# Kernel tuning notes

Measured on AMD Instinct MI355X. Metric: run time of the kernel, lower is better.

The kernel has to match this reference:

```python
import jax, jax.numpy as jnp
import numpy as np

B, N0, D, H = 64, 512, 512, 2048  # graphs, nodes/graph, d_hidden, mlp hidden


def _mlp(x, W1, b1, W2, b2, W3, b3):
    h = jax.nn.relu(x @ W1 + b1)
    h = jax.nn.relu(h @ W2 + b2)
    return h @ W3 + b3


def setup_inputs() -> dict:
    key = jax.random.key(0)
    ks = jax.random.split(key, 16)
    total = B * N0
    x = jax.random.normal(ks[0], (total, D), jnp.float32)
    node_type = jax.random.randint(ks[1], (total,), 0, 4, jnp.int32)
    action_mask = jax.random.bernoulli(ks[2], 0.5, (total,))
    node_indices = jnp.tile(jnp.arange(N0, dtype=jnp.int32), B)
    batch = jnp.repeat(jnp.arange(B, dtype=jnp.int32), N0)
    N = jnp.full((B,), N0, dtype=jnp.int32)

    def lin(k, fan_in, fan_out):
        kw, kb = jax.random.split(k)
        bound = 1.0 / np.sqrt(fan_in)
        W = jax.random.uniform(kw, (fan_in, fan_out), jnp.float32, -bound, bound)
        b = jax.random.uniform(kb, (fan_out,), jnp.float32, -bound, bound)
        return W, b

    mlp_W1, mlp_b1 = lin(ks[3], D, H)
    mlp_W2, mlp_b2 = lin(ks[4], H, H)
    mlp_W3, mlp_b3 = lin(ks[5], H, 1)
    vf_W1, vf_b1 = lin(ks[6], D, H)
    vf_W2, vf_b2 = lin(ks[7], H, H)
    vf_W3, vf_b3 = lin(ks[8], H, 1)
    return dict(x=x, node_type=node_type, action_mask=action_mask,
                node_indices=node_indices, batch=batch, N=N,
                mlp_W1=mlp_W1, mlp_b1=mlp_b1, mlp_W2=mlp_W2, mlp_b2=mlp_b2,
                mlp_W3=mlp_W3, mlp_b3=mlp_b3,
                vf_W1=vf_W1, vf_b1=vf_b1, vf_W2=vf_W2, vf_b2=vf_b2,
                vf_W3=vf_W3, vf_b3=vf_b3)


def reference(x, node_type, action_mask, node_indices, batch, N,
              mlp_W1, mlp_b1, mlp_W2, mlp_b2, mlp_W3, mlp_b3,
              vf_W1, vf_b1, vf_W2, vf_b2, vf_W3, vf_b3):
    nb = N.shape[0]
    # global mean pool over graphs
    counts = jax.ops.segment_sum(jnp.ones((x.shape[0],), x.dtype), batch, num_segments=nb)
    h_mean = jax.ops.segment_sum(x, batch, num_segments=nb) / counts[:, None]
    # masked gather -> MLP -> scatter with -inf fill, expressed as masked select
    z_node = _mlp(x, mlp_W1, mlp_b1, mlp_W2, mlp_b2, mlp_W3, mlp_b3)[:, 0]
    z_all = jnp.where(action_mask, z_node, -jnp.inf)
    z = z_all.reshape(nb, -1)  # multi_length=False: all graphs have N[0] nodes
    v = _mlp(h_mean, vf_W1, vf_b1, vf_W2, vf_b2, vf_W3, vf_b3)
    return z, v
```

## Files before the change

kernel.cpp:

```cpp
#include <hip/hip_runtime.h>
#include <cstdint>
#include <cmath>


typedef __bf16 bf16_t;
typedef float  f32x4  __attribute__((ext_vector_type(4)));
typedef int    i32x4  __attribute__((ext_vector_type(4)));
typedef int    i32x8  __attribute__((ext_vector_type(8)));

#define NB      64
#define N0      512
#define DIM     512
#define HID     2048
#define TOTAL   32768
#define ZNEG    -3.0e38f

__device__ __forceinline__ void gload16(const void* g, void* l) {
  __builtin_amdgcn_global_load_lds(
      (const uint32_t __attribute__((address_space(1)))*)g,
      (uint32_t __attribute__((address_space(3)))*)l, 16, 0, 0);
}

__device__ __forceinline__ unsigned char to_fp8(float f) {
  return (unsigned char)(__builtin_amdgcn_cvt_pk_fp8_f32(f, f, 0, false) & 0xff);
}

__global__ void mask_scan_kernel(const unsigned char* __restrict__ mask,
                                 int* __restrict__ perm,
                                 int* __restrict__ pos,
                                 int* __restrict__ mcount) {
  __shared__ int ts[1024];
  const int t = threadIdx.x;
  const uint32_t* m32 = (const uint32_t*)mask;
  uint32_t w[8];
  int s = 0;
#pragma unroll
  for (int k = 0; k < 8; ++k) {
    w[k] = m32[t * 8 + k];
    s += __popc(w[k] & 0x01010101u);
  }
  ts[t] = s;
  __syncthreads();
  for (int off = 1; off < 1024; off <<= 1) {
    int v = (t >= off) ? ts[t - off] : 0;
    __syncthreads();
    ts[t] += v;
    __syncthreads();
  }
  int run = ts[t] - s;
  const int base = t * 32;
#pragma unroll
  for (int k = 0; k < 32; ++k) {
    int bit = (w[k >> 2] >> ((k & 3) * 8)) & 1;
    if (bit) {
      perm[run] = base + k;
      pos[base + k] = run;
      run++;
    }
  }
  if (t == 1023) {
    mcount[0] = ts[1023];
    mcount[1] = (ts[1023] + 127) & ~127;
  }
}

__global__ void gather_fp8_kernel(const float* __restrict__ x,
                                  const int* __restrict__ perm,
                                  const int* __restrict__ mcount,
                                  uint32_t* __restrict__ xc) {
  const int idx = blockIdx.x * 256 + threadIdx.x;
  const int r = idx >> 7;
  const int c = idx & 127;
  if (r >= mcount[1]) return;
  uint32_t v = 0;
  if (r < mcount[0]) {
    const float4 f = ((const float4*)(x + (size_t)perm[r] * DIM))[c];
    int p = __builtin_amdgcn_cvt_pk_fp8_f32(f.x, f.y, 0, false);
    p = __builtin_amdgcn_cvt_pk_fp8_f32(f.z, f.w, p, true);
    v = (uint32_t)p;
  }
  xc[idx] = v;
}


__global__ void transpose_to_fp8_kernel(const float* __restrict__ W,
                                        uint8_t* __restrict__ Wt,
                                        int K, int N, float scale) {
  __shared__ float tile[32][33];
  const int bx = blockIdx.x;
  const int by = blockIdx.y;
  const int tx = threadIdx.x & 31;
  const int ty = threadIdx.x >> 5;
#pragma unroll
  for (int r = 0; r < 4; ++r)
    tile[ty + r * 8][tx] = W[(size_t)(by * 32 + ty + r * 8) * N + bx * 32 + tx];
  __syncthreads();
#pragma unroll
  for (int r = 0; r < 4; ++r)
    Wt[(size_t)(bx * 32 + ty + r * 8) * K + by * 32 + tx] =
        to_fp8(tile[tx][ty + r * 8] * scale);
}

__global__ void zero_kernel(float* __restrict__ p, int n) {
  int i = blockIdx.x * 256 + threadIdx.x;
  if (i < n) p[i] = 0.f;
}

__global__ void hmean_accum_kernel(const float* __restrict__ x,
                                   float* __restrict__ hsumT) {
  const int g = blockIdx.x >> 3;
  const int slab = blockIdx.x & 7;
  const int c = threadIdx.x;
  const float* xp = x + ((size_t)g * N0 + slab * 64) * DIM + c;
  float s = 0.f;
#pragma unroll 8
  for (int r = 0; r < 64; ++r) s += xp[(size_t)r * DIM];
  atomicAdd(&hsumT[(size_t)c * NB + g], s);
}

__global__ void vf_partial_kernel(const float* __restrict__ h,
                                  const float* __restrict__ W,
                                  float* __restrict__ pacc,
                                  int kspan) {
  const int tx = threadIdx.x & 31;
  const int ty = threadIdx.x >> 5;
  const int n  = blockIdx.x * 32 + tx;
  const int g0 = ty * 8;
  const int k0 = blockIdx.y * kspan;
  float acc[8] = {};
  const float* wp = W + (size_t)k0 * HID + n;
  const float* hp = h + (size_t)k0 * NB + g0;
#pragma unroll 8
  for (int kk = 0; kk < kspan; ++kk) {
    float w = wp[(size_t)kk * HID];
    float4 h0 = *(const float4*)(hp + kk * NB);
    float4 h1 = *(const float4*)(hp + kk * NB + 4);
    acc[0] += h0.x * w; acc[1] += h0.y * w;
    acc[2] += h0.z * w; acc[3] += h0.w * w;
    acc[4] += h1.x * w; acc[5] += h1.y * w;
    acc[6] += h1.z * w; acc[7] += h1.w * w;
  }
#pragma unroll
  for (int r = 0; r < 8; ++r)
    pacc[((size_t)blockIdx.y * NB + g0 + r) * HID + n] = acc[r];
}

__global__ void vf_l1_fin_kernel(const float* __restrict__ pacc1,
                                 const float* __restrict__ vb1,
                                 float* __restrict__ vh1t) {
  const int idx = blockIdx.x * 256 + threadIdx.x;
  const int g = idx >> 11;
  const int n = idx & 2047;
  float s = 0.f;
#pragma unroll
  for (int kg = 0; kg < 8; ++kg)
    s += pacc1[((size_t)kg * NB + g) * HID + n];
  vh1t[(size_t)n * NB + g] = fmaxf(s * (1.f / 512.f) + vb1[n], 0.f);
}

__global__ void vf_l23_fin_kernel(const float* __restrict__ pacc2,
                                  const float* __restrict__ vb2,
                                  const float* __restrict__ vW3,
                                  float* __restrict__ vfzp) {
  __shared__ float rs[4];
  const int g = blockIdx.x >> 3;
  const int n = (blockIdx.x & 7) * 256 + threadIdx.x;
  float s = 0.f;
#pragma unroll
  for (int kg = 0; kg < 16; ++kg)
    s += pacc2[((size_t)kg * NB + g) * HID + n];
  float t = fmaxf(s + vb2[n], 0.f) * vW3[n];
#pragma unroll
  for (int off = 32; off; off >>= 1) t += __shfl_down(t, off, 64);
  if ((threadIdx.x & 63) == 0) rs[threadIdx.x >> 6] = t;
  __syncthreads();
  if (threadIdx.x == 0)
    vfzp[g * 8 + (blockIdx.x & 7)] = rs[0] + rs[1] + rs[2] + rs[3];
}

template <int FUSE>
__global__ __launch_bounds__(256) void gemm_f8(
    const uint8_t* __restrict__ A, const uint8_t* __restrict__ Bt,
    const float* __restrict__ bias, const float* __restrict__ w3,
    uint8_t* __restrict__ C, float* __restrict__ zout,
    const int* __restrict__ mlim, int M, int N, int K, int sb) {
  const int bm = blockIdx.y;
  const int bn = blockIdx.x;
  if (bm * 128 >= *mlim) return;

  __shared__ __align__(16) char Asb[128 * 128];
  __shared__ __align__(16) char Bsb[128 * 128];

  const int tid = threadIdx.x;
  const int wave = tid >> 6;
  const int lane = tid & 63;
  const int lr = lane & 15;
  const int lq = lane >> 4;
  const int swz = lr & 7;
  const int wm = (wave >> 1) << 6;
  const int wn = (wave & 1) << 6;

  const int srow0 = (wave << 3) + (lane >> 3);
  const int gchunk = (lane & 7) ^ (lane >> 3);

  const uint8_t* ag = A + (size_t)(bm * 128 + srow0) * K + (gchunk << 4);
  const uint8_t* bg = Bt + (size_t)(bn * 128 + srow0) * K + (gchunk << 4);
  char* asw = Asb + (wave << 10);
  char* bsw = Bsb + (wave << 10);

  f32x4 acc[4][4] = {};

  for (int k0 = 0; k0 < K; k0 += 128) {
#pragma unroll
    for (int j = 0; j < 4; ++j) {
      gload16(ag + (size_t)(j * 32) * K, asw + j * 4096);
      gload16(bg + (size_t)(j * 32) * K, bsw + j * 4096);
    }
    ag += 128;
    bg += 128;
    __syncthreads();

    i32x8 a8[4], b8[4];
#pragma unroll
    for (int i = 0; i < 4; ++i) {
      const char* base = Asb + ((wm + i * 16 + lr) << 7);
      i32x4 lo = *(const i32x4*)(base + ((((lq << 1) | 0) ^ swz) << 4));
      i32x4 hi = *(const i32x4*)(base + ((((lq << 1) | 1) ^ swz) << 4));
      a8[i] = __builtin_shufflevector(lo, hi, 0, 1, 2, 3, 4, 5, 6, 7);
    }
#pragma unroll
    for (int j = 0; j < 4; ++j) {
      const char* base = Bsb + ((wn + j * 16 + lr) << 7);
      i32x4 lo = *(const i32x4*)(base + ((((lq << 1) | 0) ^ swz) << 4));
      i32x4 hi = *(const i32x4*)(base + ((((lq << 1) | 1) ^ swz) << 4));
      b8[j] = __builtin_shufflevector(lo, hi, 0, 1, 2, 3, 4, 5, 6, 7);
    }
#pragma unroll
    for (int i = 0; i < 4; ++i)
#pragma unroll
      for (int j = 0; j < 4; ++j)
        acc[i][j] = __builtin_amdgcn_mfma_scale_f32_16x16x128_f8f6f4(
            a8[i], b8[j], acc[i][j], 0 , 0 ,
            0, 127 , 0, sb);
    __syncthreads();
  }

  if (FUSE == 0) {
#pragma unroll
    for (int j = 0; j < 4; ++j) {
      const int gc = bn * 128 + wn + j * 16 + lr;
      const float bj = bias[gc];
#pragma unroll
      for (int i = 0; i < 4; ++i) {
        const int gr0 = bm * 128 + wm + i * 16 + lq * 4;
#pragma unroll
        for (int r = 0; r < 4; ++r) {
          float v = fmaxf(acc[i][j][r] + bj, 0.f);
          C[(size_t)(gr0 + r) * N + gc] = to_fp8(v);
        }
      }
    }
  } else {
    float rs[4][4] = {};
#pragma unroll
    for (int j = 0; j < 4; ++j) {
      const int gc = bn * 128 + wn + j * 16 + lr;
      const float bj = bias[gc];
      const float wj = w3[gc];
#pragma unroll
      for (int i = 0; i < 4; ++i)
#pragma unroll
        for (int r = 0; r < 4; ++r)
          rs[i][r] += fmaxf(acc[i][j][r] + bj, 0.f) * wj;
    }
#pragma unroll
    for (int off = 1; off < 16; off <<= 1) {
#pragma unroll
      for (int i = 0; i < 4; ++i)
#pragma unroll
        for (int r = 0; r < 4; ++r)
          rs[i][r] += __shfl_xor(rs[i][r], off, 64);
    }
    if (lr == 0) {
#pragma unroll
      for (int i = 0; i < 4; ++i)
#pragma unroll
        for (int r = 0; r < 4; ++r)
          atomicAdd(&zout[bm * 128 + wm + i * 16 + lq * 4 + r], rs[i][r]);
    }
  }
}

__global__ void finalize_kernel(const float* __restrict__ zp,
                                const float* __restrict__ vfzp,
                                const unsigned char* __restrict__ mask,
                                const int* __restrict__ pos,
                                const float* __restrict__ b3,
                                const float* __restrict__ vb3,
                                float* __restrict__ out) {
  int i = blockIdx.x * 256 + threadIdx.x;
  if (i < TOTAL) {
    out[i] = mask[i] ? (zp[pos[i]] + b3[0]) : ZNEG;
  } else if (i < TOTAL + NB) {
    int g = i - TOTAL;
    float v = 0.f;
#pragma unroll
    for (int b = 0; b < 8; ++b) v += vfzp[g * 8 + b];
    out[i] = v + vb3[0];
  }
}

extern "C" void kernel_launch(void* const* d_in, const int* in_sizes, int n_in,
                              void* d_out, int out_size, void* d_ws,
                              size_t ws_size, hipStream_t stream) {
  (void)in_sizes; (void)n_in; (void)out_size; (void)ws_size;
  const float* x    = (const float*)d_in[0];
  const unsigned char* mask = (const unsigned char*)d_in[2];
  const float* W1   = (const float*)d_in[6];
  const float* b1   = (const float*)d_in[7];
  const float* W2   = (const float*)d_in[8];
  const float* b2   = (const float*)d_in[9];
  const float* W3   = (const float*)d_in[10];
  const float* b3   = (const float*)d_in[11];
  const float* vW1  = (const float*)d_in[12];
  const float* vb1  = (const float*)d_in[13];
  const float* vW2  = (const float*)d_in[14];
  const float* vb2  = (const float*)d_in[15];
  const float* vW3  = (const float*)d_in[16];
  const float* vb3  = (const float*)d_in[17];
  float* out = (float*)d_out;

  char* p = (char*)d_ws;
  size_t off = 0;
  auto alloc = [&](size_t bytes) {
    void* r = p + off;
    off = (off + bytes + 255) & ~(size_t)255;
    return r;
  };
  uint8_t* x_f8  = (uint8_t*)alloc((size_t)TOTAL * DIM);
  uint8_t* W1t   = (uint8_t*)alloc((size_t)HID * DIM);
  uint8_t* W2t   = (uint8_t*)alloc((size_t)HID * HID);
  uint8_t* H1    = (uint8_t*)alloc((size_t)TOTAL * HID);
  float*   vh1t  = (float*)alloc((size_t)HID * NB * 4);
  float*   pacc1 = (float*)alloc((size_t)8 * NB * HID * 4);
  float*   pacc2 = (float*)alloc((size_t)16 * NB * HID * 4);
  float*   vfzp  = (float*)alloc((size_t)NB * 8 * 4);
  int*     perm  = (int*)alloc((size_t)TOTAL * 4);
  int*     pos   = (int*)alloc((size_t)TOTAL * 4);
  int*     mcount= (int*)alloc(256);
  float*   zreg  = (float*)alloc((size_t)(DIM * NB + TOTAL) * 4);
  float*   hsumT = zreg;
  float*   zpart = zreg + DIM * NB;

  mask_scan_kernel<<<1, 1024, 0, stream>>>(mask, perm, pos, mcount);
  gather_fp8_kernel<<<TOTAL * 128 / 256, 256, 0, stream>>>(
      x, perm, mcount, (uint32_t*)x_f8);

  transpose_to_fp8_kernel<<<dim3(HID / 32, DIM / 32), 256, 0, stream>>>(
      W1, W1t, DIM, HID, 16.f);
  transpose_to_fp8_kernel<<<dim3(HID / 32, HID / 32), 256, 0, stream>>>(
      W2, W2t, HID, HID, 32.f);
  const int nzero = DIM * NB + TOTAL;
  zero_kernel<<<(nzero + 255) / 256, 256, 0, stream>>>(zreg, nzero);

  hmean_accum_kernel<<<NB * 8, 512, 0, stream>>>(x, hsumT);

  vf_partial_kernel<<<dim3(64, 8), 256, 0, stream>>>(
      hsumT, vW1, pacc1, 64);
  vf_l1_fin_kernel<<<512, 256, 0, stream>>>(pacc1, vb1, vh1t);
  vf_partial_kernel<<<dim3(64, 16), 256, 0, stream>>>(
      vh1t, vW2, pacc2, 128);
  vf_l23_fin_kernel<<<512, 256, 0, stream>>>(pacc2, vb2, vW3, vfzp);

  gemm_f8<0><<<dim3(HID / 128, TOTAL / 128), 256, 0, stream>>>(
      x_f8, W1t, b1, nullptr, H1, nullptr, mcount + 1, TOTAL, HID, DIM, 123);
  gemm_f8<1><<<dim3(HID / 128, TOTAL / 128), 256, 0, stream>>>(
      H1, W2t, b2, W3, nullptr, zpart, mcount + 1, TOTAL, HID, HID, 122);

  finalize_kernel<<<(TOTAL + NB + 255) / 256, 256, 0, stream>>>(
      zpart, vfzp, mask, pos, b3, vb3, out);
}
```

Before: 288.9 us.

## Register-tile value-function GEMV and stage activations in LDS with finer K split

New measurement: 273.7 us. 1.06x faster.

```diff
diff --git a/kernel.cpp b/kernel.cpp
--- a/kernel.cpp
+++ b/kernel.cpp
@@ -122,27 +122,40 @@
                                   const float* __restrict__ W,
                                   float* __restrict__ pacc,
                                   int kspan) {
+  __shared__ float hs[64 * 64];
   const int tx = threadIdx.x & 31;
   const int ty = threadIdx.x >> 5;
-  const int n  = blockIdx.x * 32 + tx;
+  const int n0 = blockIdx.x * 128 + tx * 4;
   const int g0 = ty * 8;
   const int k0 = blockIdx.y * kspan;
-  float acc[8] = {};
-  const float* wp = W + (size_t)k0 * HID + n;
-  const float* hp = h + (size_t)k0 * NB + g0;
-#pragma unroll 8
+
+  const float4* hsrc = (const float4*)(h + (size_t)k0 * NB);
+  for (int i = threadIdx.x; i < (kspan << 4); i += 256)
+    ((float4*)hs)[i] = hsrc[i];
+  __syncthreads();
+
+  float acc[8][4] = {};
+  const float* wp = W + (size_t)k0 * HID + n0;
+#pragma unroll 4
   for (int kk = 0; kk < kspan; ++kk) {
-    float w = wp[(size_t)kk * HID];
-    float4 h0 = *(const float4*)(hp + kk * NB);
-    float4 h1 = *(const float4*)(hp + kk * NB + 4);
-    acc[0] += h0.x * w; acc[1] += h0.y * w;
-    acc[2] += h0.z * w; acc[3] += h0.w * w;
-    acc[4] += h1.x * w; acc[5] += h1.y * w;
-    acc[6] += h1.z * w; acc[7] += h1.w * w;
-  }
-#pragma unroll
-  for (int r = 0; r < 8; ++r)
-    pacc[((size_t)blockIdx.y * NB + g0 + r) * HID + n] = acc[r];
+    const float4 w = *(const float4*)(wp + (size_t)kk * HID);
+    const float* hr = hs + (kk << 6) + g0;
+    const float4 ha = *(const float4*)hr;
+    const float4 hb = *(const float4*)(hr + 4);
+    const float hv[8] = {ha.x, ha.y, ha.z, ha.w, hb.x, hb.y, hb.z, hb.w};
+#pragma unroll
+    for (int r = 0; r < 8; ++r) {
+      acc[r][0] += hv[r] * w.x;
+      acc[r][1] += hv[r] * w.y;
+      acc[r][2] += hv[r] * w.z;
+      acc[r][3] += hv[r] * w.w;
+    }
+  }
+#pragma unroll
+  for (int r = 0; r < 8; ++r) {
+    float4 o = {acc[r][0], acc[r][1], acc[r][2], acc[r][3]};
+    *(float4*)(pacc + ((size_t)blockIdx.y * NB + g0 + r) * HID + n0) = o;
+  }
 }
 
 __global__ void vf_l1_fin_kernel(const float* __restrict__ pacc1,
@@ -153,7 +166,7 @@
   const int n = idx & 2047;
   float s = 0.f;
 #pragma unroll
-  for (int kg = 0; kg < 8; ++kg)
+  for (int kg = 0; kg < 16; ++kg)
     s += pacc1[((size_t)kg * NB + g) * HID + n];
   vh1t[(size_t)n * NB + g] = fmaxf(s * (1.f / 512.f) + vb1[n], 0.f);
 }
@@ -167,7 +180,7 @@
   const int n = (blockIdx.x & 7) * 256 + threadIdx.x;
   float s = 0.f;
 #pragma unroll
-  for (int kg = 0; kg < 16; ++kg)
+  for (int kg = 0; kg < 32; ++kg)
     s += pacc2[((size_t)kg * NB + g) * HID + n];
   float t = fmaxf(s + vb2[n], 0.f) * vW3[n];
 #pragma unroll
@@ -342,8 +355,8 @@
   uint8_t* W2t   = (uint8_t*)alloc((size_t)HID * HID);
   uint8_t* H1    = (uint8_t*)alloc((size_t)TOTAL * HID);
   float*   vh1t  = (float*)alloc((size_t)HID * NB * 4);
-  float*   pacc1 = (float*)alloc((size_t)8 * NB * HID * 4);
-  float*   pacc2 = (float*)alloc((size_t)16 * NB * HID * 4);
+  float*   pacc1 = (float*)alloc((size_t)16 * NB * HID * 4);
+  float*   pacc2 = (float*)alloc((size_t)32 * NB * HID * 4);
   float*   vfzp  = (float*)alloc((size_t)NB * 8 * 4);
   int*     perm  = (int*)alloc((size_t)TOTAL * 4);
   int*     pos   = (int*)alloc((size_t)TOTAL * 4);
@@ -365,11 +378,11 @@
 
   hmean_accum_kernel<<<NB * 8, 512, 0, stream>>>(x, hsumT);
 
-  vf_partial_kernel<<<dim3(64, 8), 256, 0, stream>>>(
-      hsumT, vW1, pacc1, 64);
+  vf_partial_kernel<<<dim3(16, 16), 256, 0, stream>>>(
+      hsumT, vW1, pacc1, 32);
   vf_l1_fin_kernel<<<512, 256, 0, stream>>>(pacc1, vb1, vh1t);
-  vf_partial_kernel<<<dim3(64, 16), 256, 0, stream>>>(
-      vh1t, vW2, pacc2, 128);
+  vf_partial_kernel<<<dim3(16, 32), 256, 0, stream>>>(
+      vh1t, vW2, pacc2, 64);
   vf_l23_fin_kernel<<<512, 256, 0, stream>>>(pacc2, vb2, vW3, vfzp);
 
   gemm_f8<0><<<dim3(HID / 128, TOTAL / 128), 256, 0, stream>>>(
```
